# Kernel tuning notes

Measured on AMD Instinct MI355X. Metric: run time of the kernel, lower is better.

## Reference

```python
import jax, jax.numpy as jnp
import numpy as np
from jax import lax

BN_EPS = 1e-5


def _condconv(x, w, b, fc_w, fc_b):
    """CondConv2D: per-sample expert mixing then 3x3 conv (pad=1, stride=1).
    x: [B, Cin, H, W]; w: [E, Cout, Cin, 3, 3]; b: [Cout]; fc_w: [E, Cin]; fc_b: [E].
    """
    B, Cin, H, W = x.shape
    E, Cout, _, kh, kw = w.shape
    pooled = x.mean(axis=(2, 3))                               # [B, Cin] adaptive_avg_pool2d(1,1)+flatten
    rw = jax.nn.sigmoid(pooled @ fc_w.T + fc_b)                # [B, E] routing weights
    kernels = jnp.einsum('be,eoihw->boihw', rw, w)             # [B, Cout, Cin, 3, 3]
    # Batched per-sample conv via grouped conv: groups = B
    xi = x.reshape(1, B * Cin, H, W)
    ker = kernels.reshape(B * Cout, Cin, kh, kw)
    out = lax.conv_general_dilated(
        xi, ker, window_strides=(1, 1), padding=((1, 1), (1, 1)),
        feature_group_count=B,
        dimension_numbers=('NCHW', 'OIHW', 'NCHW'))
    return out.reshape(B, Cout, H, W) + b[None, :, None, None]


def _bn_relu(x, g, b, m, v):
    # eval-mode BatchNorm2d followed by ReLU
    inv = g * lax.rsqrt(v + BN_EPS)
    return jax.nn.relu(x * inv[None, :, None, None] + (b - m * inv)[None, :, None, None])


def setup_inputs() -> dict:
    key = jax.random.key(0)
    ks = jax.random.split(key, 8)
    B, Cin, Cout, H, W, E = 16, 64, 128, 128, 128, 3
    s1 = 1.0 / np.sqrt(Cin * 9)
    s2 = 1.0 / np.sqrt(Cout * 9)
    return {
        'x': jax.random.normal(ks[0], (B, Cin, H, W), jnp.float32),
        'w1': jax.random.normal(ks[1], (E, Cout, Cin, 3, 3), jnp.float32) * s1,
        'b1': jax.random.normal(ks[2], (Cout,), jnp.float32) * s1,
        'fc1_w': jax.random.normal(ks[3], (E, Cin), jnp.float32) / np.sqrt(Cin),
        'fc1_b': jnp.zeros((E,), jnp.float32),
        'bn1_g': jnp.ones((Cout,), jnp.float32),
        'bn1_b': jnp.zeros((Cout,), jnp.float32),
        'bn1_m': jnp.zeros((Cout,), jnp.float32),
        'bn1_v': jnp.ones((Cout,), jnp.float32),
        'w2': jax.random.normal(ks[4], (E, Cout, Cout, 3, 3), jnp.float32) * s2,
        'b2': jax.random.normal(ks[5], (Cout,), jnp.float32) * s2,
        'fc2_w': jax.random.normal(ks[6], (E, Cout), jnp.float32) / np.sqrt(Cout),
        'fc2_b': jnp.zeros((E,), jnp.float32),
        'bn2_g': jnp.ones((Cout,), jnp.float32),
        'bn2_b': jnp.zeros((Cout,), jnp.float32),
        'bn2_m': jnp.zeros((Cout,), jnp.float32),
        'bn2_v': jnp.ones((Cout,), jnp.float32),
    }


def reference(x, w1, b1, fc1_w, fc1_b, bn1_g, bn1_b, bn1_m, bn1_v,
              w2, b2, fc2_w, fc2_b, bn2_g, bn2_b, bn2_m, bn2_v):
    h = _condconv(x, w1, b1, fc1_w, fc1_b)
    h = _bn_relu(h, bn1_g, bn1_b, bn1_m, bn1_v)
    h = _condconv(h, w2, b2, fc2_w, fc2_b)
    h = _bn_relu(h, bn2_g, bn2_b, bn2_m, bn2_v)
    return h
```

## Files before the change

### kernel.cpp

```cpp
#include <hip/hip_runtime.h>
#include <math.h>

#define BN_EPS 1e-5f

typedef short bf16x8 __attribute__((ext_vector_type(8)));
typedef float f32x4 __attribute__((ext_vector_type(4)));
typedef float f32x16 __attribute__((ext_vector_type(16)));
typedef unsigned short ushort8v __attribute__((ext_vector_type(8)));
typedef unsigned int uint;
typedef unsigned short ushort;

__device__ inline ushort f2bf(float f) {
    uint u = __float_as_uint(f);
    uint r = u + 0x7FFFu + ((u >> 16) & 1u);
    return (ushort)(r >> 16);
}
__device__ inline float bf2f(ushort u) { return __uint_as_float(((uint)u) << 16); }

__global__ void scsh_kernel(const float* b1, const float* g1, const float* bb1,
                            const float* m1, const float* v1,
                            const float* b2, const float* g2, const float* bb2,
                            const float* m2, const float* v2,
                            float* scsh1, float* scsh2) {
    int t = threadIdx.x;
    if (t < 128) {
        float sc = g1[t] * rsqrtf(v1[t] + BN_EPS);
        scsh1[t] = sc;
        scsh1[128 + t] = (b1[t] - m1[t]) * sc + bb1[t];
    } else {
        int c = t - 128;
        float sc = g2[c] * rsqrtf(v2[c] + BN_EPS);
        scsh2[c] = sc;
        scsh2[128 + c] = (b2[c] - m2[c]) * sc + bb2[c];
    }
}

__global__ void xprep_kernel(const float* __restrict__ x, ushort* __restrict__ xT,
                             float* __restrict__ pooled1) {
    __shared__ float t[64][65];
    const int b = blockIdx.y;
    const int p0 = blockIdx.x * 64;
    const int tid = threadIdx.x;
#pragma unroll
    for (int it = 0; it < 16; ++it) {
        const int idx = it * 256 + tid;
        const int ci = idx >> 6, p = idx & 63;
        t[ci][p] = x[((size_t)b * 64 + ci) * 16384 + p0 + p];
    }
    __syncthreads();
    const int h = p0 >> 7;
#pragma unroll
    for (int it = 0; it < 2; ++it) {
        const int p = it * 32 + (tid >> 3);
        const int w = (p0 & 127) + p;
        const int c0 = (tid & 7) * 8;
        const int cc = c0 >> 4;
        ushort8v u;
#pragma unroll
        for (int j = 0; j < 8; ++j) u[j] = f2bf(t[c0 + j][p]);
        *(ushort8v*)&xT[(((size_t)(b * 128 + h) * 4 + cc) * 128 + w) * 16 + (c0 & 15)] = u;
    }
    if (tid < 64) {
        float s = 0.f;
#pragma unroll 8
        for (int p = 0; p < 64; ++p) s += t[tid][p];
        atomicAdd(&pooled1[b * 64 + tid], s);
    }
}

__global__ void pool2h_kernel(const ushort* __restrict__ hT, float* __restrict__ pooled2) {
    const int b = blockIdx.x, slab = blockIdx.y;
    const int tid = threadIdx.x;
    const int cc = tid >> 5, o = (tid >> 4) & 1, wb = tid & 15;
    float a[8] = {0.f, 0.f, 0.f, 0.f, 0.f, 0.f, 0.f, 0.f};
    for (int r = 0; r < 4; ++r) {
        const int h = slab * 4 + r;
        const ushort* base = hT + ((size_t)(b * 128 + h) * 8 + cc) * 2048 + o * 8;
#pragma unroll
        for (int k = 0; k < 8; ++k) {
            const ushort8v u = *(const ushort8v*)(base + (wb + k * 16) * 16);
#pragma unroll
            for (int j = 0; j < 8; ++j) a[j] += bf2f(u[j]);
        }
    }
    __shared__ float sp[16][8][17];
    const int grp0 = cc * 2 + o;
#pragma unroll
    for (int j = 0; j < 8; ++j) sp[grp0][j][wb] = a[j];
    __syncthreads();
    if (tid < 128) {
        const int grp = tid >> 3, j = tid & 7;
        float s = 0.f;
#pragma unroll
        for (int k = 0; k < 16; ++k) s += sp[grp][j][k];
        const int c = (grp >> 1) * 16 + (grp & 1) * 8 + j;
        atomicAdd(&pooled2[b * 128 + c], s);
    }
}

template <int CIN>
__global__ void mix_route_kernel(const float* __restrict__ w, const float* __restrict__ pooled,
                                 const float* __restrict__ fcw, const float* __restrict__ fcb,
                                 ushort* __restrict__ wmix) {
    constexpr int NCC = CIN / 16;
    __shared__ float rwl[48];
    const int tid = threadIdx.x;
    if (tid < 48) {
        const int bb = tid / 3, e = tid % 3;
        float d = 0.f;
        for (int c = 0; c < CIN; ++c) d += pooled[bb * CIN + c] * fcw[e * CIN + c];
        const float s = fcb[e] + d * (1.f / 16384.f);
        rwl[tid] = 1.f / (1.f + expf(-s));
    }
    __syncthreads();
    const int co = blockIdx.x;
    const int sw = (co >> 2) & 1;
    for (int b = 0; b < 16; ++b) {
        const float r0 = rwl[b * 3 + 0], r1 = rwl[b * 3 + 1], r2 = rwl[b * 3 + 2];
        for (int idx = tid; idx < CIN * 9; idx += 256) {
            const int ci = idx & (CIN - 1);
            const int tap = idx / CIN;
            const size_t off = ((size_t)co * CIN + ci) * 9 + tap;
            const float m = r0 * w[off]
                          + r1 * w[off + (size_t)128 * CIN * 9]
                          + r2 * w[off + (size_t)2 * 128 * CIN * 9];
            const int cc = ci >> 4, o = (ci >> 3) & 1, e = ci & 7;
            const size_t dst = (((size_t)(b * NCC + cc)) * 2304
                             + (tap * 128 + co) * 2 + (o ^ sw)) * 8 + e;
            wmix[dst] = f2bf(m);
        }
    }
}

template <int CIN, bool TO_BF16>
__global__ __launch_bounds__(512, 2)
void conv_mfma5_kernel(const ushort* __restrict__ xT, const ushort* __restrict__ wmix,
                       const float* __restrict__ scsh,
                       float* __restrict__ outf, ushort* __restrict__ outh) {
    constexpr int NCC = CIN / 16;
    constexpr int IBUF = 24960;
    constexpr int WOFF = 2 * IBUF;
    constexpr int WBUF = 36864;
    __shared__ __align__(16) char smem[123648];

    const int L = ((blockIdx.x & 7) << 6) | (blockIdx.x >> 3);
    const int b = L >> 5;
    const int rt = L & 31;

    const int tid = threadIdx.x;
    const int lane = tid & 63, wid = tid >> 6;
    const int wm = wid >> 2, wn = wid & 3;
    const int l31 = lane & 31, lhi = lane >> 5;

    f32x16 acc[2][4];
#pragma unroll
    for (int i = 0; i < 2; ++i)
#pragma unroll
        for (int j = 0; j < 4; ++j)
#pragma unroll
            for (int r = 0; r < 16; ++r) acc[i][j][r] = 0.f;

    const ushort* inb = xT + (size_t)b * 128 * NCC * 2048;
    const ushort* wmb = wmix + (size_t)b * NCC * 18432;

    auto stage = [&](int bufi, int cc) {
        const ushort* wsrc = wmb + (size_t)cc * 18432;
        for (int j = wid; j < 60; j += 8) {
            if (j < 24) {
                const int r = j >> 2, i = j & 3;
                const int hg = rt * 4 - 1 + r;
                if ((unsigned)hg < 128u) {
                    const int q = i * 64 + lane;
                    const int cm1 = q >> 1;
                    const int so = (q & 1) ^ (((cm1 + 1) >> 2) & 1);
                    const ushort* src = inb + ((size_t)(hg * NCC + cc)) * 2048 + cm1 * 16 + so * 8;
                    __builtin_amdgcn_global_load_lds(
                        (const __attribute__((address_space(1))) void*)src,
                        (__attribute__((address_space(3))) void*)(smem + bufi * IBUF + (r * 260 + 2 + i * 64) * 16),
                        16, 0, 0);
                }
            } else {
                const int k = j - 24;
                const ushort* src = wsrc + k * 512 + lane * 8;
                __builtin_amdgcn_global_load_lds(
                    (const __attribute__((address_space(1))) void*)src,
                    (__attribute__((address_space(3))) void*)(smem + WOFF + bufi * WBUF + k * 1024),
                    16, 0, 0);
            }
        }
    };

    auto taps = [&](int bufi) {
        const char* ldsI = smem + bufi * IBUF;
        const char* ldsW = smem + WOFF + bufi * WBUF;
#pragma unroll
        for (int tap = 0; tap < 9; ++tap) {
            const int dy = tap / 3, dx = tap - dy * 3;
            bf16x8 af[2];
#pragma unroll
            for (int mf = 0; mf < 2; ++mf) {
                const int co = wm * 64 + mf * 32 + l31;
                const int g = (tap * 128 + co) * 2 + (lhi ^ ((co >> 2) & 1));
                af[mf] = *(const bf16x8*)(ldsW + g * 16);
            }
#pragma unroll
            for (int nf = 0; nf < 4; ++nf) {
                const int col = nf * 32 + l31 + dx;
                const int g = (wn + dy) * 260 + col * 2 + (lhi ^ ((col >> 2) & 1));
                const bf16x8 bv = *(const bf16x8*)(ldsI + g * 16);
#pragma unroll
                for (int mf = 0; mf < 2; ++mf)
                    acc[mf][nf] = __builtin_amdgcn_mfma_f32_32x32x16_bf16(
                        af[mf], bv, acc[mf][nf], 0, 0, 0);
            }
        }
    };

    if (tid < 48) {
        const int bi = tid & 1, idx = tid >> 1;
        const int r = idx >> 2, e = idx & 3;
        const int rem = (e < 2) ? e : 256 + e;
        *(f32x4*)(smem + bi * IBUF + (r * 260 + rem) * 16) = f32x4{0.f, 0.f, 0.f, 0.f};
    }
    if (rt == 0 || rt == 31) {
        const int r = (rt == 0) ? 0 : 5;
        for (int g = tid; g < 520; g += 512) {
            const int bi = (g >= 260) ? 1 : 0, gr = g - bi * 260;
            *(f32x4*)(smem + bi * IBUF + (r * 260 + gr) * 16) = f32x4{0.f, 0.f, 0.f, 0.f};
        }
    }

    stage(0, 0);
    asm volatile("s_waitcnt vmcnt(0)" ::: "memory");
    __syncthreads();

    for (int cc = 0; cc < NCC; ++cc) {
        if (cc + 1 < NCC) stage((cc & 1) ^ 1, cc + 1);
        __builtin_amdgcn_sched_barrier(0);
        taps(cc & 1);
        __syncthreads();
    }

    if constexpr (!TO_BF16) {
#pragma unroll
        for (int mf = 0; mf < 2; ++mf) {
            const int cob = wm * 64 + mf * 32 + 4 * lhi;
            f32x4 sc[4], sh[4];
#pragma unroll
            for (int q = 0; q < 4; ++q) {
                sc[q] = *(const f32x4*)&scsh[cob + 8 * q];
                sh[q] = *(const f32x4*)&scsh[128 + cob + 8 * q];
            }
#pragma unroll
            for (int nf = 0; nf < 4; ++nf) {
                const size_t pbase = (size_t)(rt * 4 + wn) * 128 + nf * 32 + l31;
#pragma unroll
                for (int q = 0; q < 4; ++q)
#pragma unroll
                    for (int s = 0; s < 4; ++s) {
                        float y = fmaf(acc[mf][nf][q * 4 + s], sc[q][s], sh[q][s]);
                        y = y > 0.f ? y : 0.f;
                        outf[((size_t)(b * 128 + cob + 8 * q + s)) * 16384 + pbase] = y;
                    }
            }
        }
    } else {
        ushort* sf = (ushort*)smem;
#pragma unroll
        for (int p = 0; p < 2; ++p) {
            if ((wn >> 1) == p) {
                const int lr = wn & 1;
#pragma unroll
                for (int mf = 0; mf < 2; ++mf)
#pragma unroll
                    for (int q = 0; q < 4; ++q) {
                        const int co4 = wm * 64 + mf * 32 + 8 * q + 4 * lhi;
                        const f32x4 sc = *(const f32x4*)&scsh[co4];
                        const f32x4 sh = *(const f32x4*)&scsh[128 + co4];
#pragma unroll
                        for (int nf = 0; nf < 4; ++nf) {
                            const int px = lr * 128 + nf * 32 + l31;
                            float v[4];
#pragma unroll
                            for (int s = 0; s < 4; ++s) {
                                float y = fmaf(acc[mf][nf][q * 4 + s], sc[s], sh[s]);
                                v[s] = y > 0.f ? y : 0.f;
                            }
                            uint2 pk;
                            pk.x = (uint)f2bf(v[0]) | ((uint)f2bf(v[1]) << 16);
                            pk.y = (uint)f2bf(v[2]) | ((uint)f2bf(v[3]) << 16);
                            *(uint2*)&sf[px * 136 + co4] = pk;
                        }
                    }
            }
            __syncthreads();
#pragma unroll
            for (int it = 0; it < 4; ++it) {
                const int id = it * 512 + tid;
                const int lr = id >> 10, cc = (id >> 7) & 7, w = id & 127;
                const uint4 v0 = *(const uint4*)&sf[(lr * 128 + w) * 136 + cc * 16];
                const uint4 v1 = *(const uint4*)&sf[(lr * 128 + w) * 136 + cc * 16 + 8];
                ushort* dst = outh + (((size_t)(b * 128 + rt * 4 + 2 * p + lr)) * 8 + cc) * 2048 + w * 16;
                *(uint4*)dst = v0;
                *(uint4*)(dst + 8) = v1;
            }
            if (p == 0) __syncthreads();
        }
    }
}

extern "C" void kernel_launch(void* const* d_in, const int* in_sizes, int n_in,
                              void* d_out, int out_size, void* d_ws, size_t ws_size,
                              hipStream_t stream) {
    const float* x     = (const float*)d_in[0];
    const float* w1    = (const float*)d_in[1];
    const float* b1    = (const float*)d_in[2];
    const float* fc1_w = (const float*)d_in[3];
    const float* fc1_b = (const float*)d_in[4];
    const float* bn1g  = (const float*)d_in[5];
    const float* bn1b  = (const float*)d_in[6];
    const float* bn1m  = (const float*)d_in[7];
    const float* bn1v  = (const float*)d_in[8];
    const float* w2    = (const float*)d_in[9];
    const float* b2    = (const float*)d_in[10];
    const float* fc2_w = (const float*)d_in[11];
    const float* fc2_b = (const float*)d_in[12];
    const float* bn2g  = (const float*)d_in[13];
    const float* bn2b  = (const float*)d_in[14];
    const float* bn2m  = (const float*)d_in[15];
    const float* bn2v  = (const float*)d_in[16];

    float* out = (float*)d_out;
    char* ws = (char*)d_ws;

    ushort* hT    = (ushort*)(ws + 0);
    ushort* xT    = (ushort*)(ws + 67108864);
    ushort* wmix1 = (ushort*)(ws + 100663296);
    ushort* wmix2 = (ushort*)(ws + 103022592);
    float*  pool1 = (float*) (ws + 107741184);
    float*  pool2 = (float*) (ws + 107745280);
    float*  scsh1 = (float*) (ws + 107753472);
    float*  scsh2 = (float*) (ws + 107754496);

    hipMemsetAsync(pool1, 0, 4096, stream);
    hipMemsetAsync(pool2, 0, 8192, stream);

    scsh_kernel<<<1, 256, 0, stream>>>(b1, bn1g, bn1b, bn1m, bn1v,
                                       b2, bn2g, bn2b, bn2m, bn2v, scsh1, scsh2);

    xprep_kernel<<<dim3(256, 16), 256, 0, stream>>>(x, xT, pool1);
    mix_route_kernel<64><<<128, 256, 0, stream>>>(w1, pool1, fc1_w, fc1_b, wmix1);
    conv_mfma5_kernel<64, true><<<512, 512, 0, stream>>>(
        xT, wmix1, scsh1, nullptr, hT);

    pool2h_kernel<<<dim3(16, 32), 256, 0, stream>>>(hT, pool2);
    mix_route_kernel<128><<<128, 256, 0, stream>>>(w2, pool2, fc2_w, fc2_b, wmix2);
    conv_mfma5_kernel<128, false><<<512, 512, 0, stream>>>(
        hT, wmix2, scsh2, out, nullptr);
}
```

Baseline: 213.4 us.

## Fuse layer-2 pooling into conv epilogue, restructure staging, add setprio and packed bf16 cvt

Removes the separate pool2h pass by accumulating the post-ReLU channel sums in the first conv's epilogue. The sums are reduced across the wave with shuffles and committed with atomics, which saves a full reread of the bf16 intermediate. The LDS staging loop is rewritten with precomputed offsets and unrolled fixed trip counts, and the sched_barrier is dropped. MFMA sections get raised wave priority via s_setprio, and the bf16 packing uses the hardware v_cvt_pk_bf16_f32 instruction. Atomics add contention to the epilogue, and the pooled sums now come from fp32 values rather than bf16-rounded ones.

```diff
diff --git a/kernel.cpp b/kernel.cpp
--- a/kernel.cpp
+++ b/kernel.cpp
@@ -16,6 +16,11 @@
     return (ushort)(r >> 16);
 }
 __device__ inline float bf2f(ushort u) { return __uint_as_float(((uint)u) << 16); }
+__device__ inline uint cvtpk(float lo, float hi) {
+    uint r;
+    asm("v_cvt_pk_bf16_f32 %0, %1, %2" : "=v"(r) : "v"(lo), "v"(hi));
+    return r;
+}
 
 __global__ void scsh_kernel(const float* b1, const float* g1, const float* bb1,
                             const float* m1, const float* v1,
@@ -65,36 +70,6 @@
 #pragma unroll 8
         for (int p = 0; p < 64; ++p) s += t[tid][p];
         atomicAdd(&pooled1[b * 64 + tid], s);
-    }
-}
-
-__global__ void pool2h_kernel(const ushort* __restrict__ hT, float* __restrict__ pooled2) {
-    const int b = blockIdx.x, slab = blockIdx.y;
-    const int tid = threadIdx.x;
-    const int cc = tid >> 5, o = (tid >> 4) & 1, wb = tid & 15;
-    float a[8] = {0.f, 0.f, 0.f, 0.f, 0.f, 0.f, 0.f, 0.f};
-    for (int r = 0; r < 4; ++r) {
-        const int h = slab * 4 + r;
-        const ushort* base = hT + ((size_t)(b * 128 + h) * 8 + cc) * 2048 + o * 8;
-#pragma unroll
-        for (int k = 0; k < 8; ++k) {
-            const ushort8v u = *(const ushort8v*)(base + (wb + k * 16) * 16);
-#pragma unroll
-            for (int j = 0; j < 8; ++j) a[j] += bf2f(u[j]);
-        }
-    }
-    __shared__ float sp[16][8][17];
-    const int grp0 = cc * 2 + o;
-#pragma unroll
-    for (int j = 0; j < 8; ++j) sp[grp0][j][wb] = a[j];
-    __syncthreads();
-    if (tid < 128) {
-        const int grp = tid >> 3, j = tid & 7;
-        float s = 0.f;
-#pragma unroll
-        for (int k = 0; k < 16; ++k) s += sp[grp][j][k];
-        const int c = (grp >> 1) * 16 + (grp & 1) * 8 + j;
-        atomicAdd(&pooled2[b * 128 + c], s);
     }
 }
 
@@ -134,9 +109,10 @@
 
 template <int CIN, bool TO_BF16>
 __global__ __launch_bounds__(512, 2)
-void conv_mfma5_kernel(const ushort* __restrict__ xT, const ushort* __restrict__ wmix,
+void conv_mfma6_kernel(const ushort* __restrict__ xT, const ushort* __restrict__ wmix,
                        const float* __restrict__ scsh,
-                       float* __restrict__ outf, ushort* __restrict__ outh) {
+                       float* __restrict__ outf, ushort* __restrict__ outh,
+                       float* __restrict__ pool2) {
     constexpr int NCC = CIN / 16;
     constexpr int IBUF = 24960;
     constexpr int WOFF = 2 * IBUF;
@@ -163,28 +139,35 @@
     const ushort* inb = xT + (size_t)b * 128 * NCC * 2048;
     const ushort* wmb = wmix + (size_t)b * NCC * 18432;
 
+    const int iq   = (wid & 3) * 64 + lane;
+    const int icm  = iq >> 1;
+    const int iso  = (iq & 1) ^ (((icm + 1) >> 2) & 1);
+    const int voff_in = icm * 16 + iso * 8;
+    const int hg0     = rt * 4 - 1 + (wid >> 2);
+    const int dsti0   = ((wid >> 2) * 260 + 2 + (wid & 3) * 64) * 16;
+    const int wsoff  = wid * 512 + lane * 8;
+    const int wdst0  = WOFF + wid * 1024;
+
     auto stage = [&](int bufi, int cc) {
-        const ushort* wsrc = wmb + (size_t)cc * 18432;
-        for (int j = wid; j < 60; j += 8) {
-            if (j < 24) {
-                const int r = j >> 2, i = j & 3;
-                const int hg = rt * 4 - 1 + r;
-                if ((unsigned)hg < 128u) {
-                    const int q = i * 64 + lane;
-                    const int cm1 = q >> 1;
-                    const int so = (q & 1) ^ (((cm1 + 1) >> 2) & 1);
-                    const ushort* src = inb + ((size_t)(hg * NCC + cc)) * 2048 + cm1 * 16 + so * 8;
-                    __builtin_amdgcn_global_load_lds(
-                        (const __attribute__((address_space(1))) void*)src,
-                        (__attribute__((address_space(3))) void*)(smem + bufi * IBUF + (r * 260 + 2 + i * 64) * 16),
-                        16, 0, 0);
-                }
-            } else {
-                const int k = j - 24;
-                const ushort* src = wsrc + k * 512 + lane * 8;
+        const int ccoff = cc * 2048;
+#pragma unroll
+        for (int u = 0; u < 3; ++u) {
+            const int hg = hg0 + 2 * u;
+            if ((unsigned)hg < 128u) {
+                const ushort* src = inb + (size_t)hg * (NCC * 2048) + ccoff + voff_in;
                 __builtin_amdgcn_global_load_lds(
                     (const __attribute__((address_space(1))) void*)src,
-                    (__attribute__((address_space(3))) void*)(smem + WOFF + bufi * WBUF + k * 1024),
+                    (__attribute__((address_space(3))) void*)(smem + bufi * IBUF + dsti0 + u * 8320),
+                    16, 0, 0);
+            }
+        }
+        const ushort* wsrc = wmb + (size_t)cc * 18432 + wsoff;
+#pragma unroll
+        for (int u = 0; u < 5; ++u) {
+            if (wid + u * 8 < 36) {
+                __builtin_amdgcn_global_load_lds(
+                    (const __attribute__((address_space(1))) void*)(wsrc + u * 4096),
+                    (__attribute__((address_space(3))) void*)(smem + bufi * WBUF + wdst0 + u * 8192),
                     16, 0, 0);
             }
         }
@@ -193,6 +176,7 @@
     auto taps = [&](int bufi) {
         const char* ldsI = smem + bufi * IBUF;
         const char* ldsW = smem + WOFF + bufi * WBUF;
+        __builtin_amdgcn_s_setprio(1);
 #pragma unroll
         for (int tap = 0; tap < 9; ++tap) {
             const int dy = tap / 3, dx = tap - dy * 3;
@@ -214,6 +198,7 @@
                         af[mf], bv, acc[mf][nf], 0, 0, 0);
             }
         }
+        __builtin_amdgcn_s_setprio(0);
     };
 
     if (tid < 48) {
@@ -236,7 +221,6 @@
 
     for (int cc = 0; cc < NCC; ++cc) {
         if (cc + 1 < NCC) stage((cc & 1) ^ 1, cc + 1);
-        __builtin_amdgcn_sched_barrier(0);
         taps(cc & 1);
         __syncthreads();
     }
@@ -277,6 +261,7 @@
                         const int co4 = wm * 64 + mf * 32 + 8 * q + 4 * lhi;
                         const f32x4 sc = *(const f32x4*)&scsh[co4];
                         const f32x4 sh = *(const f32x4*)&scsh[128 + co4];
+                        float ps0 = 0.f, ps1 = 0.f, ps2 = 0.f, ps3 = 0.f;
 #pragma unroll
                         for (int nf = 0; nf < 4; ++nf) {
                             const int px = lr * 128 + nf * 32 + l31;
@@ -286,10 +271,24 @@
                                 float y = fmaf(acc[mf][nf][q * 4 + s], sc[s], sh[s]);
                                 v[s] = y > 0.f ? y : 0.f;
                             }
+                            ps0 += v[0]; ps1 += v[1]; ps2 += v[2]; ps3 += v[3];
                             uint2 pk;
-                            pk.x = (uint)f2bf(v[0]) | ((uint)f2bf(v[1]) << 16);
-                            pk.y = (uint)f2bf(v[2]) | ((uint)f2bf(v[3]) << 16);
+                            pk.x = cvtpk(v[0], v[1]);
+                            pk.y = cvtpk(v[2], v[3]);
                             *(uint2*)&sf[px * 136 + co4] = pk;
+                        }
+#pragma unroll
+                        for (int m = 1; m <= 16; m <<= 1) {
+                            ps0 += __shfl_xor(ps0, m);
+                            ps1 += __shfl_xor(ps1, m);
+                            ps2 += __shfl_xor(ps2, m);
+                            ps3 += __shfl_xor(ps3, m);
+                        }
+                        if (l31 == 0) {
+                            atomicAdd(&pool2[b * 128 + co4 + 0], ps0);
+                            atomicAdd(&pool2[b * 128 + co4 + 1], ps1);
+                            atomicAdd(&pool2[b * 128 + co4 + 2], ps2);
+                            atomicAdd(&pool2[b * 128 + co4 + 3], ps3);
                         }
                     }
             }
@@ -350,11 +349,10 @@
 
     xprep_kernel<<<dim3(256, 16), 256, 0, stream>>>(x, xT, pool1);
     mix_route_kernel<64><<<128, 256, 0, stream>>>(w1, pool1, fc1_w, fc1_b, wmix1);
-    conv_mfma5_kernel<64, true><<<512, 512, 0, stream>>>(
-        xT, wmix1, scsh1, nullptr, hT);
-
-    pool2h_kernel<<<dim3(16, 32), 256, 0, stream>>>(hT, pool2);
+    conv_mfma6_kernel<64, true><<<512, 512, 0, stream>>>(
+        xT, wmix1, scsh1, nullptr, hT, pool2);
+
     mix_route_kernel<128><<<128, 256, 0, stream>>>(w2, pool2, fc2_w, fc2_b, wmix2);
-    conv_mfma5_kernel<128, false><<<512, 512, 0, stream>>>(
-        hT, wmix2, scsh2, out, nullptr);
-}
+    conv_mfma6_kernel<128, false><<<512, 512, 0, stream>>>(
+        hT, wmix2, scsh2, out, nullptr, nullptr);
+}
```

Measured after the change: 229.8 us. 1.08x slower.
